# Performance work log

Measured on AMD Instinct MI355X. Metric: run time of the kernel, lower is better.

The kernel has to match this reference:

```python
import jax, jax.numpy as jnp
import numpy as np
from jax import lax

N_HARM = 64
N_BINS = 64
SR = 16000
B, T = 16, 64000


def setup_inputs() -> dict:
    key = jax.random.key(0)
    ks = jax.random.split(key, 12)
    audio = jax.random.normal(ks[0], (B, T), dtype=jnp.float32)
    # realistic fundamental frequencies in [80, 400) Hz
    f0 = 80.0 + 320.0 * jax.random.uniform(ks[1], (B, T), dtype=jnp.float32)
    white_noise = jax.random.normal(ks[2], (B, T), dtype=jnp.float32)
    def wconv(k, o, i, ksz):
        return jax.random.normal(k, (o, i, ksz), dtype=jnp.float32) * (1.0 / np.sqrt(i * ksz))
    w1 = wconv(ks[3], 32, 1, 9); b1 = jnp.zeros((32,), jnp.float32)
    w2 = wconv(ks[4], 64, 32, 9); b2 = jnp.zeros((64,), jnp.float32)
    w3 = wconv(ks[5], 128, 64, 9); b3 = jnp.zeros((128,), jnp.float32)
    wl = jax.random.normal(ks[6], (N_HARM + N_BINS, 128), dtype=jnp.float32) * (1.0 / np.sqrt(128))
    bl = jnp.zeros((N_HARM + N_BINS,), jnp.float32)
    return {"audio": audio, "f0": f0, "white_noise": white_noise,
            "w1": w1, "b1": b1, "w2": w2, "b2": b2, "w3": w3, "b3": b3,
            "wl": wl, "bl": bl}


def _conv1d(x, w, b):
    # x: [B, C_in, T], w: [C_out, C_in, K]; stride 2, pad 4
    y = lax.conv_general_dilated(x, w, window_strides=(2,), padding=[(4, 4)],
                                 dimension_numbers=("NCH", "OIH", "NCH"))
    return jax.nn.relu(y + b[None, :, None])


def reference(audio, f0, white_noise, w1, b1, w2, b2, w3, b3, wl, bl):
    batch, time = audio.shape
    # --- encoder ---
    x = audio[:, None, :]                    # [B, 1, T]
    x = _conv1d(x, w1, b1)                   # [B, 32, T/2]
    x = _conv1d(x, w2, b2)                   # [B, 64, T/4]
    x = _conv1d(x, w3, b3)                   # [B, 128, T/8]
    pooled = x.mean(axis=2)                  # AdaptiveAvgPool1d(1) + Flatten -> [B, 128]
    feats = pooled @ wl.T + bl               # [B, 128]
    # --- harmonic synth ---
    amps = jax.nn.relu(feats[:, :N_HARM])    # [B, H]; constant over time in original
    amps = amps / (amps.sum(axis=1, keepdims=True) + 1e-6)
    t = jnp.linspace(0.0, time / SR, time)   # endpoint-inclusive, as torch.linspace
    harm_idx = jnp.arange(1, N_HARM + 1, dtype=jnp.float32)
    # phase: [B, H, T] = 2*pi * (h * f0) * t
    phase = (2.0 * jnp.pi) * f0[:, None, :] * harm_idx[None, :, None] * t[None, None, :]
    harmonic_audio = jnp.einsum("bh,bht->bt", amps, jnp.sin(phase))
    # --- noise synth ---
    noise_mag = feats[:, N_HARM:]            # [B, n_bins]; mean over time of a constant = itself
    bin_size = time // N_BINS
    shaped = (white_noise.reshape(batch, N_BINS, bin_size) * noise_mag[:, :, None]).reshape(batch, time)
    return harmonic_audio + shaped
```

## Files before the change

kernel.cpp:

```cpp
#include <hip/hip_runtime.h>
#include <hip/hip_bf16.h>
#include <math.h>

typedef unsigned short u16;
typedef _Float16 f16x2 __attribute__((ext_vector_type(2)));
typedef _Float16 f16x8 __attribute__((ext_vector_type(8)));
typedef float    f32x16 __attribute__((ext_vector_type(16)));
typedef u16      u16x8  __attribute__((ext_vector_type(8)));
typedef u16      u16x4  __attribute__((ext_vector_type(4)));

#define BATCH 16
#define T0 64000
#define T1 32000
#define T2 16000
#define T3 8000
#define NT3 250
#define NBLKX 32
#define NROWS1 1040

static __device__ __forceinline__ u16 f2h(float f) {
    _Float16 h = (_Float16)f;
    u16 u;
    __builtin_memcpy(&u, &h, 2);
    return u;
}

__global__ __launch_bounds__(256) void prep_w_k(const float* __restrict__ w1,
                                                const float* __restrict__ b1,
                                                const float* __restrict__ w2,
                                                const float* __restrict__ w3,
                                                u16* __restrict__ w1p,
                                                u16* __restrict__ a2t,
                                                u16* __restrict__ a3t,
                                                int* __restrict__ cnt) {
    int idx = blockIdx.x * 256 + threadIdx.x;
    if (idx < 18432) {
        int j = idx & 7, o = (idx >> 3) & 63, g = (idx >> 9) & 3, kk = idx >> 11;
        a2t[idx] = f2h(w2[(o * 32 + g * 8 + j) * 9 + kk]);
    } else if (idx < 18432 + 73728) {
        int jdx = idx - 18432;
        int j = jdx & 7, o = (jdx >> 3) & 127, g = (jdx >> 10) & 7, kk = jdx >> 13;
        a3t[jdx] = f2h(w3[(o * 64 + g * 8 + j) * 9 + kk]);
    } else if (idx < 18432 + 73728 + 16) {
        cnt[idx - 18432 - 73728] = 0;
    } else if (idx < 18432 + 73728 + 16 + 160) {
        int j = idx - (18432 + 73728 + 16);
        int ch = j / 5, q = j % 5;
        float a = (q < 4) ? w1[ch * 9 + 2 * q]     : w1[ch * 9 + 8];
        float b = (q < 4) ? w1[ch * 9 + 2 * q + 1] : b1[ch];
        f16x2 pk;
        pk[0] = (_Float16)a;
        pk[1] = (_Float16)b;
        *(f16x2*)(w1p + 2 * j) = pk;
    }
}

__global__ __launch_bounds__(512, 2) void mega_k(const float* __restrict__ audio,
                                                 const float* __restrict__ w1,
                                                 const float* __restrict__ b1,
                                                 const u16* __restrict__ w1p,
                                                 const u16* __restrict__ a2t,
                                                 const float* __restrict__ b2,
                                                 const u16* __restrict__ a3t,
                                                 const float* __restrict__ b3,
                                                 float* __restrict__ partials,
                                                 int* __restrict__ cnt,
                                                 const float* __restrict__ wl,
                                                 const float* __restrict__ bl,
                                                 float* __restrict__ featbuf) {
    __shared__ u16 sm[520 * 64];
    const int tid = threadIdx.x;
    const int b = blockIdx.y;
    const int r0 = blockIdx.x * NT3;
    const int lane = tid & 63, wv = tid >> 6;
    const int ls = lane >> 5, ln = lane & 31;

    {
        const float* ar = audio + (size_t)b * T0;
        const bool edge = (blockIdx.x == 0) || (blockIdx.x == NBLKX - 1);
        const f16x2* wp = (const f16x2*)w1p;
        #pragma unroll
        for (int rep = 0; rep < 3; ++rep) {
            int l1 = rep * 512 + tid;
            if (l1 >= NROWS1) break;
            int t1 = 4 * r0 - 12 + l1;
            int rr = l1 >> 1, pp = l1 & 1;
            if (edge) {
                if (t1 < 0 || t1 >= T1) {
                    u16x8 z;
                    #pragma unroll
                    for (int q = 0; q < 8; ++q) z[q] = 0;
                    #pragma unroll
                    for (int g = 0; g < 4; ++g) {
                        int slot = (pp * 4 + g) ^ (rr & 7);
                        *(u16x8*)(sm + rr * 64 + slot * 8) = z;
                    }
                } else {
                    int base = 2 * t1 - 4;
                    float x[9];
                    #pragma unroll
                    for (int k = 0; k < 9; ++k) {
                        int t0v = base + k;
                        x[k] = (t0v >= 0 && t0v < T0) ? ar[t0v] : 0.f;
                    }
                    #pragma unroll
                    for (int g = 0; g < 4; ++g) {
                        u16x8 v;
                        #pragma unroll
                        for (int j = 0; j < 8; ++j) {
                            int ch = g * 8 + j;
                            float acc = b1[ch];
                            #pragma unroll
                            for (int k = 0; k < 9; ++k) acc = fmaf(x[k], w1[ch * 9 + k], acc);
                            v[j] = f2h(fmaxf(acc, 0.f));
                        }
                        int slot = (pp * 4 + g) ^ (rr & 7);
                        *(u16x8*)(sm + rr * 64 + slot * 8) = v;
                    }
                }
            } else {
                int base = 2 * t1 - 4;
                f16x2 xp[5];
                {
                    const float2* p2 = (const float2*)(ar + base);
                    #pragma unroll
                    for (int q = 0; q < 4; ++q) {
                        float2 c = p2[q];
                        xp[q][0] = (_Float16)c.x;
                        xp[q][1] = (_Float16)c.y;
                    }
                    float x8v = ar[base + 8];
                    xp[4][0] = (_Float16)x8v;
                    xp[4][1] = (_Float16)1.0f;
                }
                #pragma unroll
                for (int g = 0; g < 4; ++g) {
                    f16x8 vv;
                    #pragma unroll
                    for (int jp = 0; jp < 4; ++jp) {
                        int ch0 = g * 8 + 2 * jp;
                        float a0 = 0.f, a1 = 0.f;
                        #pragma unroll
                        for (int q = 0; q < 5; ++q) {
                            a0 = __builtin_amdgcn_fdot2(xp[q], wp[ch0 * 5 + q], a0, false);
                            a1 = __builtin_amdgcn_fdot2(xp[q], wp[(ch0 + 1) * 5 + q], a1, false);
                        }
                        vv[2 * jp]     = (_Float16)fmaxf(a0, 0.f);
                        vv[2 * jp + 1] = (_Float16)fmaxf(a1, 0.f);
                    }
                    int slot = (pp * 4 + g) ^ (rr & 7);
                    *(f16x8*)(sm + rr * 64 + slot * 8) = vv;
                }
            }
        }
    }
    __syncthreads();

    for (int cc = 0; cc < 2; ++cc) {
        int nl = cc * 256 + 32 * wv + ln;
        f32x16 acc2[2];
        #pragma unroll
        for (int mi = 0; mi < 2; ++mi)
            #pragma unroll
            for (int q = 0; q < 16; ++q) acc2[mi][q] = 0.f;
        f16x8 bfB[2];
        #pragma unroll 3
        for (int kk = 0; kk < 9; ++kk) {
            {
                int rr = nl + (kk >> 1);
                int pp = kk & 1;
                #pragma unroll
                for (int step = 0; step < 2; ++step) {
                    int slot = (pp * 4 + 2 * step + ls) ^ (rr & 7);
                    bfB[step] = *(const f16x8*)(sm + rr * 64 + slot * 8);
                }
            }
            const u16* ap = a2t + kk * 2048;
            #pragma unroll
            for (int step = 0; step < 2; ++step) {
                f16x8 af0 = *(const f16x8*)(ap + (2 * step + ls) * 512 + ln * 8);
                f16x8 af1 = *(const f16x8*)(ap + (2 * step + ls) * 512 + (32 + ln) * 8);
                acc2[0] = __builtin_amdgcn_mfma_f32_32x32x16_f16(af0, bfB[step], acc2[0], 0, 0, 0);
                acc2[1] = __builtin_amdgcn_mfma_f32_32x32x16_f16(af1, bfB[step], acc2[1], 0, 0, 0);
            }
        }
        __syncthreads();
        int l2 = nl;
        int t2 = 2 * r0 - 4 + l2;
        bool valid = (t2 >= 0) && (t2 < T2);
        #pragma unroll
        for (int mi = 0; mi < 2; ++mi)
            #pragma unroll
            for (int q = 0; q < 4; ++q) {
                u16x4 v;
                #pragma unroll
                for (int d = 0; d < 4; ++d) {
                    int o = 32 * mi + 8 * q + 4 * ls + d;
                    float xv = valid ? fmaxf(acc2[mi][4 * q + d] + b2[o], 0.f) : 0.f;
                    v[d] = f2h(xv);
                }
                int gy = 4 * mi + q;
                int sy = gy ^ ((l2 >> 1) & 7);
                *(u16x4*)(sm + l2 * 64 + sy * 8 + ls * 4) = v;
            }
        __syncthreads();
    }

    const int mh = wv & 1, nh = wv >> 1;
    f32x16 acc3[2][2];
    #pragma unroll
    for (int mi = 0; mi < 2; ++mi)
        #pragma unroll
        for (int ni = 0; ni < 2; ++ni)
            #pragma unroll
            for (int q = 0; q < 16; ++q) acc3[mi][ni][q] = 0.f;

    f16x8 bf[2][4];
    #pragma unroll 3
    for (int kk = 0; kk < 9; ++kk) {
        const u16* ap = a3t + kk * 8192;
        {
            #pragma unroll
            for (int ni = 0; ni < 2; ++ni) {
                int nl = 64 * nh + 32 * ni + ln;
                int l2 = 2 * nl + kk;
                int rrC = nl + (kk >> 1);
                #pragma unroll
                for (int step = 0; step < 4; ++step) {
                    int sy = (2 * step + ls) ^ (rrC & 7);
                    bf[ni][step] = *(const f16x8*)(sm + l2 * 64 + sy * 8);
                }
            }
        }
        #pragma unroll
        for (int step = 0; step < 4; ++step) {
            f16x8 af0 = *(const f16x8*)(ap + (2 * step + ls) * 1024 + (64 * mh + ln) * 8);
            f16x8 af1 = *(const f16x8*)(ap + (2 * step + ls) * 1024 + (64 * mh + 32 + ln) * 8);
            #pragma unroll
            for (int ni = 0; ni < 2; ++ni) {
                acc3[0][ni] = __builtin_amdgcn_mfma_f32_32x32x16_f16(af0, bf[ni][step], acc3[0][ni], 0, 0, 0);
                acc3[1][ni] = __builtin_amdgcn_mfma_f32_32x32x16_f16(af1, bf[ni][step], acc3[1][ni], 0, 0, 0);
            }
        }
    }

    float loc[32];
    #pragma unroll
    for (int mi = 0; mi < 2; ++mi)
        #pragma unroll
        for (int r = 0; r < 16; ++r) {
            int o = 64 * mh + 32 * mi + (r & 3) + 8 * (r >> 2) + 4 * ls;
            float bias = b3[o];
            float s = 0.f;
            #pragma unroll
            for (int ni = 0; ni < 2; ++ni) {
                int nl = 64 * nh + 32 * ni + ln;
                float v = fmaxf(acc3[mi][ni][r] + bias, 0.f);
                s += (nl < NT3) ? v : 0.f;
            }
            loc[mi * 16 + r] = s;
        }
    __syncthreads();
    float* smf = (float*)sm;
    #pragma unroll
    for (int mi = 0; mi < 2; ++mi)
        #pragma unroll
        for (int r = 0; r < 16; ++r) {
            int o = 64 * mh + 32 * mi + (r & 3) + 8 * (r >> 2) + 4 * ls;
            smf[nh * 4096 + o * 32 + ln] = loc[mi * 16 + r];
        }
    __syncthreads();
    if (tid < 128) {
        int o = tid;
        float s = 0.f;
        #pragma unroll
        for (int j = 0; j < 32; ++j) {
            int col = (j + o) & 31;
            s += smf[o * 32 + col] + smf[4096 + o * 32 + col]
               + smf[8192 + o * 32 + col] + smf[12288 + o * 32 + col];
        }
        __hip_atomic_store(&partials[((size_t)b * NBLKX + blockIdx.x) * 128 + o], s,
                           __ATOMIC_RELAXED, __HIP_MEMORY_SCOPE_AGENT);
    }

    __syncthreads();
    int* smi = (int*)sm;
    if (tid == 0) {
        int done = atomicAdd(&cnt[b], 1);
        smi[0] = (done == NBLKX - 1) ? 1 : 0;
    }
    __syncthreads();
    if (smi[0]) {
        float* pr = (float*)sm + 64;
        {
            int o = tid & 127, sub = tid >> 7;
            const float* base = partials + (size_t)b * NBLKX * 128 + o;
            float s = 0.f;
            #pragma unroll
            for (int q = 0; q < 8; ++q)
                s += __hip_atomic_load(base + (sub + 4 * q) * 128,
                                       __ATOMIC_RELAXED, __HIP_MEMORY_SCOPE_AGENT);
            pr[sub * 128 + o] = s;
        }
        __syncthreads();
        float* pl = (float*)sm + 64 + 512;
        float* fl = (float*)sm + 64 + 512 + 128;
        if (tid < 128)
            pl[tid] = (pr[tid] + pr[128 + tid] + pr[256 + tid] + pr[384 + tid])
                      * (1.0f / (float)T3);
        __syncthreads();
        {
            int o = tid >> 2, sub = tid & 3;
            const float4* wp4 = (const float4*)(wl + o * 128 + sub * 32);
            const float4* pp4 = (const float4*)(pl + sub * 32);
            float s = 0.f;
            #pragma unroll
            for (int q = 0; q < 8; ++q) {
                float4 w4 = wp4[q];
                float4 p4 = pp4[q];
                s += w4.x * p4.x + w4.y * p4.y + w4.z * p4.z + w4.w * p4.w;
            }
            s += __shfl_xor(s, 1);
            s += __shfl_xor(s, 2);
            if (sub == 0) fl[o] = s + bl[o];
        }
        __syncthreads();
        if (tid < 128) {
            float feat = fl[tid];
            if (tid < 64) {
                float r = fmaxf(feat, 0.f);
                float ssum = r;
                #pragma unroll
                for (int off = 32; off > 0; off >>= 1) ssum += __shfl_xor(ssum, off);
                featbuf[b * 128 + tid] = r / (ssum + 1e-6f);
            } else {
                featbuf[b * 128 + tid] = feat;
            }
        }
    }
}

__global__ __launch_bounds__(256) void synth_k(const float* __restrict__ f0,
                                               const float* __restrict__ wn,
                                               const float* __restrict__ featbuf,
                                               float* __restrict__ out) {
    const int tid = threadIdx.x;
    const int b = blockIdx.y;
    __shared__ float sa[64];
    __shared__ float nm[64];
    if (tid < 64) sa[tid] = featbuf[b * 128 + tid];
    else if (tid < 128) nm[tid - 64] = featbuf[b * 128 + tid];
    __syncthreads();

    const int t0v = blockIdx.x * 1024 + tid * 4;
    if (t0v >= T0) return;

    const float4 fv = *(const float4*)(f0 + (size_t)b * T0 + t0v);
    const float4 wv = *(const float4*)(wn + (size_t)b * T0 + t0v);

    float sc[4], sp[4], tc[4], ac[4];
    #pragma unroll
    for (int s = 0; s < 4; ++s) {
        double u = (double)((&fv.x)[s]) * ((double)(t0v + s) * (4.0 / 63999.0));
        float uf = (float)(u - floor(u));
        sc[s] = __builtin_amdgcn_sinf(uf);
        tc[s] = 2.0f * __builtin_amdgcn_cosf(uf);
        sp[s] = 0.f;
        ac[s] = 0.f;
    }
    #pragma unroll
    for (int h = 0; h < 64; ++h) {
        float a = sa[h];
        #pragma unroll
        for (int s = 0; s < 4; ++s) {
            ac[s] = fmaf(a, sc[s], ac[s]);
            float sn = fmaf(tc[s], sc[s], -sp[s]);
            sp[s] = sc[s];
            sc[s] = sn;
        }
    }
    float4 o;
    #pragma unroll
    for (int s = 0; s < 4; ++s)
        (&o.x)[s] = ac[s] + (&wv.x)[s] * nm[(t0v + s) / 1000];
    *(float4*)(out + (size_t)b * T0 + t0v) = o;
}

extern "C" void kernel_launch(void* const* d_in, const int* in_sizes, int n_in,
                              void* d_out, int out_size, void* d_ws, size_t ws_size,
                              hipStream_t stream) {
    const float* audio = (const float*)d_in[0];
    const float* f0    = (const float*)d_in[1];
    const float* wn    = (const float*)d_in[2];
    const float* w1    = (const float*)d_in[3];
    const float* b1    = (const float*)d_in[4];
    const float* w2    = (const float*)d_in[5];
    const float* b2    = (const float*)d_in[6];
    const float* w3    = (const float*)d_in[7];
    const float* b3    = (const float*)d_in[8];
    const float* wl    = (const float*)d_in[9];
    const float* bl    = (const float*)d_in[10];
    float* out = (float*)d_out;

    char* ws = (char*)d_ws;
    int*   cnt      = (int*)(ws);
    float* featbuf  = (float*)(ws + 1024);
    u16*   w1p      = (u16*)(ws + 12288);
    u16*   a2t      = (u16*)(ws + 16384);
    u16*   a3t      = (u16*)(ws + 16384 + 36864);
    float* partials = (float*)(ws + 16384 + 36864 + 147456);

    prep_w_k<<<361, 256, 0, stream>>>(w1, b1, w2, w3, w1p, a2t, a3t, cnt);
    mega_k<<<dim3(NBLKX, BATCH), 512, 0, stream>>>(audio, w1, b1, w1p, a2t, b2, a3t, b3,
                                                   partials, cnt, wl, bl, featbuf);
    synth_k<<<dim3((T0 + 1023) / 1024, BATCH), 256, 0, stream>>>(f0, wn, featbuf, out);
}
```

Baseline: 129.5 us.

## Fuse synth stage into encoder megakernel with per-batch flag spin-wait

```diff
diff --git a/kernel.cpp b/kernel.cpp
--- a/kernel.cpp
+++ b/kernel.cpp
@@ -32,7 +32,8 @@
                                                 u16* __restrict__ w1p,
                                                 u16* __restrict__ a2t,
                                                 u16* __restrict__ a3t,
-                                                int* __restrict__ cnt) {
+                                                int* __restrict__ cnt,
+                                                int* __restrict__ flag) {
     int idx = blockIdx.x * 256 + threadIdx.x;
     if (idx < 18432) {
         int j = idx & 7, o = (idx >> 3) & 63, g = (idx >> 9) & 3, kk = idx >> 11;
@@ -43,8 +44,10 @@
         a3t[jdx] = f2h(w3[(o * 64 + g * 8 + j) * 9 + kk]);
     } else if (idx < 18432 + 73728 + 16) {
         cnt[idx - 18432 - 73728] = 0;
-    } else if (idx < 18432 + 73728 + 16 + 160) {
-        int j = idx - (18432 + 73728 + 16);
+    } else if (idx < 18432 + 73728 + 32) {
+        flag[idx - 18432 - 73728 - 16] = 0;
+    } else if (idx < 18432 + 73728 + 32 + 160) {
+        int j = idx - (18432 + 73728 + 32);
         int ch = j / 5, q = j % 5;
         float a = (q < 4) ? w1[ch * 9 + 2 * q]     : w1[ch * 9 + 8];
         float b = (q < 4) ? w1[ch * 9 + 2 * q + 1] : b1[ch];
@@ -65,9 +68,13 @@
                                                  const float* __restrict__ b3,
                                                  float* __restrict__ partials,
                                                  int* __restrict__ cnt,
+                                                 int* __restrict__ flag,
                                                  const float* __restrict__ wl,
                                                  const float* __restrict__ bl,
-                                                 float* __restrict__ featbuf) {
+                                                 float* __restrict__ featbuf,
+                                                 const float* __restrict__ f0,
+                                                 const float* __restrict__ wn,
+                                                 float* __restrict__ out) {
     __shared__ u16 sm[520 * 64];
     const int tid = threadIdx.x;
     const int b = blockIdx.y;
@@ -327,63 +334,76 @@
         __syncthreads();
         if (tid < 128) {
             float feat = fl[tid];
+            float res;
             if (tid < 64) {
                 float r = fmaxf(feat, 0.f);
                 float ssum = r;
                 #pragma unroll
                 for (int off = 32; off > 0; off >>= 1) ssum += __shfl_xor(ssum, off);
-                featbuf[b * 128 + tid] = r / (ssum + 1e-6f);
+                res = r / (ssum + 1e-6f);
             } else {
-                featbuf[b * 128 + tid] = feat;
-            }
-        }
-    }
-}
-
-__global__ __launch_bounds__(256) void synth_k(const float* __restrict__ f0,
-                                               const float* __restrict__ wn,
-                                               const float* __restrict__ featbuf,
-                                               float* __restrict__ out) {
-    const int tid = threadIdx.x;
-    const int b = blockIdx.y;
-    __shared__ float sa[64];
-    __shared__ float nm[64];
-    if (tid < 64) sa[tid] = featbuf[b * 128 + tid];
-    else if (tid < 128) nm[tid - 64] = featbuf[b * 128 + tid];
-    __syncthreads();
-
-    const int t0v = blockIdx.x * 1024 + tid * 4;
-    if (t0v >= T0) return;
-
-    const float4 fv = *(const float4*)(f0 + (size_t)b * T0 + t0v);
-    const float4 wv = *(const float4*)(wn + (size_t)b * T0 + t0v);
-
-    float sc[4], sp[4], tc[4], ac[4];
-    #pragma unroll
-    for (int s = 0; s < 4; ++s) {
-        double u = (double)((&fv.x)[s]) * ((double)(t0v + s) * (4.0 / 63999.0));
-        float uf = (float)(u - floor(u));
-        sc[s] = __builtin_amdgcn_sinf(uf);
-        tc[s] = 2.0f * __builtin_amdgcn_cosf(uf);
-        sp[s] = 0.f;
-        ac[s] = 0.f;
-    }
-    #pragma unroll
-    for (int h = 0; h < 64; ++h) {
-        float a = sa[h];
-        #pragma unroll
-        for (int s = 0; s < 4; ++s) {
-            ac[s] = fmaf(a, sc[s], ac[s]);
-            float sn = fmaf(tc[s], sc[s], -sp[s]);
-            sp[s] = sc[s];
-            sc[s] = sn;
-        }
-    }
-    float4 o;
-    #pragma unroll
-    for (int s = 0; s < 4; ++s)
-        (&o.x)[s] = ac[s] + (&wv.x)[s] * nm[(t0v + s) / 1000];
-    *(float4*)(out + (size_t)b * T0 + t0v) = o;
+                res = feat;
+            }
+            __hip_atomic_store(&featbuf[b * 128 + tid], res,
+                               __ATOMIC_RELAXED, __HIP_MEMORY_SCOPE_AGENT);
+        }
+        __syncthreads();
+        if (tid == 0)
+            __hip_atomic_store(&flag[b], 1,
+                               __ATOMIC_RELAXED, __HIP_MEMORY_SCOPE_AGENT);
+    } else {
+        if (tid == 0) {
+            while (__hip_atomic_load(&flag[b], __ATOMIC_RELAXED,
+                                     __HIP_MEMORY_SCOPE_AGENT) == 0)
+                __builtin_amdgcn_s_sleep(1);
+        }
+    }
+    __syncthreads();
+
+    {
+        float* sa = (float*)sm + 1024;
+        float* nm = (float*)sm + 1088;
+        if (tid < 64)
+            sa[tid] = __hip_atomic_load(&featbuf[b * 128 + tid],
+                                        __ATOMIC_RELAXED, __HIP_MEMORY_SCOPE_AGENT);
+        else if (tid < 128)
+            nm[tid - 64] = __hip_atomic_load(&featbuf[b * 128 + tid],
+                                             __ATOMIC_RELAXED, __HIP_MEMORY_SCOPE_AGENT);
+        __syncthreads();
+
+        if (tid < 500) {
+            const int t0v = blockIdx.x * 2000 + tid * 4;
+            const float4 fv = *(const float4*)(f0 + (size_t)b * T0 + t0v);
+            const float4 wv4 = *(const float4*)(wn + (size_t)b * T0 + t0v);
+
+            float sc[4], sp[4], tc[4], ac[4];
+            #pragma unroll
+            for (int s = 0; s < 4; ++s) {
+                double u = (double)((&fv.x)[s]) * ((double)(t0v + s) * (4.0 / 63999.0));
+                float uf = (float)(u - floor(u));
+                sc[s] = __builtin_amdgcn_sinf(uf);
+                tc[s] = 2.0f * __builtin_amdgcn_cosf(uf);
+                sp[s] = 0.f;
+                ac[s] = 0.f;
+            }
+            #pragma unroll
+            for (int h = 0; h < 64; ++h) {
+                float a = sa[h];
+                #pragma unroll
+                for (int s = 0; s < 4; ++s) {
+                    ac[s] = fmaf(a, sc[s], ac[s]);
+                    float sn = fmaf(tc[s], sc[s], -sp[s]);
+                    sp[s] = sc[s];
+                    sc[s] = sn;
+                }
+            }
+            float4 o;
+            #pragma unroll
+            for (int s = 0; s < 4; ++s)
+                (&o.x)[s] = ac[s] + (&wv4.x)[s] * nm[(t0v + s) / 1000];
+            *(float4*)(out + (size_t)b * T0 + t0v) = o;
+        }
+    }
 }
 
 extern "C" void kernel_launch(void* const* d_in, const int* in_sizes, int n_in,
@@ -404,14 +424,15 @@
 
     char* ws = (char*)d_ws;
     int*   cnt      = (int*)(ws);
+    int*   flag     = (int*)(ws + 64);
     float* featbuf  = (float*)(ws + 1024);
     u16*   w1p      = (u16*)(ws + 12288);
     u16*   a2t      = (u16*)(ws + 16384);
     u16*   a3t      = (u16*)(ws + 16384 + 36864);
     float* partials = (float*)(ws + 16384 + 36864 + 147456);
 
-    prep_w_k<<<361, 256, 0, stream>>>(w1, b1, w2, w3, w1p, a2t, a3t, cnt);
+    prep_w_k<<<361, 256, 0, stream>>>(w1, b1, w2, w3, w1p, a2t, a3t, cnt, flag);
     mega_k<<<dim3(NBLKX, BATCH), 512, 0, stream>>>(audio, w1, b1, w1p, a2t, b2, a3t, b3,
-                                                   partials, cnt, wl, bl, featbuf);
-    synth_k<<<dim3((T0 + 1023) / 1024, BATCH), 256, 0, stream>>>(f0, wn, featbuf, out);
+                                                   partials, cnt, flag, wl, bl, featbuf,
+                                                   f0, wn, out);
 }
```

Result: slower. 140.3 us (+8.3%).
